# Optimization experiments

Hardware: AMD Instinct MI355X
Metric: run time of the kernel (lower is better)

The kernel has to match this reference:

```python
import jax, jax.numpy as jnp
import numpy as np

B, D, E, H = 2048, 1024, 32, 1024  # tokens, hidden, total experts (m*N), ffn_dim_small


def setup_inputs() -> dict:
    key = jax.random.key(0)
    ks = jax.random.split(key, 5)
    scale_in = 1.0 / np.sqrt(D)
    scale_h = 1.0 / np.sqrt(H)
    return {
        "x": jax.random.normal(ks[0], (B, D), dtype=jnp.float32),
        "Wg": jax.random.normal(ks[1], (D, E), dtype=jnp.float32) * scale_in,
        "W1": jax.random.normal(ks[2], (E, D, H), dtype=jnp.float32) * scale_in,
        "b1": jnp.zeros((E, H), dtype=jnp.float32),
        "W2": jax.random.normal(ks[3], (E, H, D), dtype=jnp.float32) * scale_h,
        "b2": jnp.zeros((E, D), dtype=jnp.float32),
        "topk": 8,  # m * K
    }


def reference(x, Wg, W1, b1, W2, b2, topk):
    # gating: softmax then keep only top-k probs (others zeroed), no renorm
    logits = x @ Wg                                   # [B, E]
    probs = jax.nn.softmax(logits, axis=-1)           # [B, E]
    _, idx = jax.lax.top_k(probs, topk)               # [B, topk]
    mask = jnp.zeros_like(probs).at[jnp.arange(x.shape[0])[:, None], idx].set(1.0)
    gate = probs * mask                               # [B, E]

    # dense all-expert FFN (faithful to original which runs every expert)
    h = jax.nn.relu(jnp.einsum('bd,edh->beh', x, W1) + b1)   # [B, E, H]
    y = jnp.einsum('beh,ehd->bed', h, W2) + b2               # [B, E, D]

    moe_out = jnp.einsum('be,bed->bd', gate, y)              # weighted sum over experts
    return x + moe_out
```

## Files before the change

### kernel.cpp

```cpp
#include <hip/hip_runtime.h>
#include <hip/hip_bf16.h>

#define B_TOK 2048
#define DDIM 1024
#define NEXP 32
#define HDIM 1024
#define TOPK 8
#define PITCH 1088

typedef __bf16 bf16_t;
typedef __bf16 bf16x8 __attribute__((ext_vector_type(8)));
typedef float f32x4 __attribute__((ext_vector_type(4)));

__global__ __launch_bounds__(256) void k_prep(const float* __restrict__ x,
                                              bf16_t* __restrict__ xb) {
  int i = (blockIdx.x * 256 + threadIdx.x) * 8;
  float4 v0 = *(const float4*)&x[i];
  float4 v1 = *(const float4*)&x[i + 4];
  bf16x8 v;
  v[0] = (bf16_t)v0.x; v[1] = (bf16_t)v0.y; v[2] = (bf16_t)v0.z; v[3] = (bf16_t)v0.w;
  v[4] = (bf16_t)v1.x; v[5] = (bf16_t)v1.y; v[6] = (bf16_t)v1.z; v[7] = (bf16_t)v1.w;
  int row = i >> 10, col = i & 1023;
  *(bf16x8*)&xb[(size_t)row * PITCH + col] = v;
}

__global__ __launch_bounds__(256) void k_gating(const float* __restrict__ x,
                                                const float* __restrict__ Wg,
                                                int* __restrict__ sel_e,
                                                float* __restrict__ sel_w) {
  int token = blockIdx.x * 4 + (threadIdx.x >> 6);
  int lane = threadIdx.x & 63;
  int e = lane & 31;
  int half = lane >> 5;
  const float* xr = x + (size_t)token * DDIM + half * (DDIM / 2);
  const float* wg = Wg + (size_t)half * (DDIM / 2) * NEXP + e;
  float acc = 0.f;
#pragma unroll 8
  for (int k = 0; k < DDIM / 2; ++k) acc = fmaf(xr[k], wg[k * NEXP], acc);
  acc += __shfl_xor(acc, 32);
  float m = acc;
  for (int off = 16; off; off >>= 1) m = fmaxf(m, __shfl_xor(m, off));
  float p = __expf(acc - m);
  float s = p;
  for (int off = 16; off; off >>= 1) s += __shfl_xor(s, off);
  p /= s;
  float pv = p;
  int my_se = 0;
  float my_sw = 0.f;
  for (int it = 0; it < TOPK; ++it) {
    float mx = pv;
    for (int off = 16; off; off >>= 1) mx = fmaxf(mx, __shfl_xor(mx, off));
    unsigned long long bal = __ballot(pv == mx);
    int sl = __ffsll(bal) - 1;
    int se = sl & 31;
    if (lane == it) { my_se = se; my_sw = mx; }
    if (e == se) pv = -1.f;
  }
  if (lane < TOPK) {
    sel_e[token * TOPK + lane] = my_se;
    sel_w[token * TOPK + lane] = my_sw;
  }
}

__global__ __launch_bounds__(256) void k_build_lists(const int* __restrict__ sel_e,
                                                     const float* __restrict__ sel_w,
                                                     int* __restrict__ list,
                                                     float* __restrict__ wlist,
                                                     int* __restrict__ count) {
  int e = blockIdx.x;
  int t = threadIdx.x;
  int lane = t & 63, wv = t >> 6;
  __shared__ int wsum[4];
  __shared__ int base;
  if (t == 0) base = 0;
  __syncthreads();
  for (int c = 0; c < B_TOK; c += 256) {
    int b = c + t;
    int flag = 0, slot = 0;
    float w = 0.f;
#pragma unroll
    for (int j = 0; j < TOPK; ++j) {
      if (sel_e[b * TOPK + j] == e) { flag = 1; slot = j; w = sel_w[b * TOPK + j]; }
    }
    unsigned long long bal = __ballot(flag);
    int pre = __popcll(bal & ((1ull << lane) - 1ull));
    int tot = __popcll(bal);
    if (lane == 0) wsum[wv] = tot;
    __syncthreads();
    int off = base;
    for (int i = 0; i < wv; ++i) off += wsum[i];
    if (flag) {
      int pos = off + pre;
      list[e * B_TOK + pos] = (b << 3) | slot;
      wlist[e * B_TOK + pos] = w;
    }
    __syncthreads();
    if (t == 0) base += wsum[0] + wsum[1] + wsum[2] + wsum[3];
    __syncthreads();
  }
  if (t == 0) count[e] = base;
}

__global__ __launch_bounds__(64) void k_build_queue(const int* __restrict__ count,
                                                    int* __restrict__ queue,
                                                    int* __restrict__ qn) {
  int e = threadIdx.x;
  int nmt = 0;
  if (e < NEXP) nmt = (count[e] + 127) >> 7;
  int pref = 0, tot = 0;
  for (int i = 0; i < NEXP; ++i) {
    int v = __shfl(nmt, i);
    if (i < e) pref += v;
    tot += v;
  }
  if (e < NEXP) {
    int base = pref * 8;
    for (int y = 0; y < 8; ++y)
      for (int mt = 0; mt < nmt; ++mt)
        queue[base + y * nmt + mt] = (e << 8) | (mt << 3) | y;
  }
  if (threadIdx.x == 0) qn[0] = tot * 8;
}

__global__ __launch_bounds__(256) void k_reduce(const float* __restrict__ x,
                                               const float* __restrict__ ybuf,
                                               float* __restrict__ out) {
  int i = (blockIdx.x * 256 + threadIdx.x) * 4;
  int tok = i >> 10;
  int d = i & 1023;
  float4 s = *(const float4*)&x[i];
  const float* yb = ybuf + (size_t)tok * 8 * 1024 + d;
#pragma unroll
  for (int sl = 0; sl < 8; ++sl) {
    float4 v = *(const float4*)&yb[sl * 1024];
    s.x += v.x; s.y += v.y; s.z += v.z; s.w += v.w;
  }
  *(float4*)&out[i] = s;
}

__device__ __forceinline__ void async_load16(const bf16_t* g, bf16_t* l) {
  __builtin_amdgcn_global_load_lds((const __attribute__((address_space(1))) void*)g,
                                   (__attribute__((address_space(3))) void*)l, 16, 0, 0);
}

#define LOADB(LO, HI, KT)                                                     \
  {                                                                           \
    const float* p_ = bcol + (size_t)((KT)*64 + aB * 8) * 1024;               \
    _Pragma("unroll") for (int kk = 0; kk < 8; ++kk) {                        \
      LO[kk] = *(const float2*)(p_ + (size_t)kk * 1024);                      \
      HI[kk] = *(const float2*)(p_ + (size_t)kk * 1024 + 64);                 \
    }                                                                         \
  }

#define CVTWRITE(LO, HI)                                                      \
  {                                                                           \
    _Pragma("unroll") for (int jn = 0; jn < 4; ++jn) {                        \
      const int n = (jn < 2) ? (2 * qB + jn) : (64 + 2 * qB + (jn - 2));      \
      bf16x8 pk;                                                              \
      _Pragma("unroll") for (int kk = 0; kk < 8; ++kk)                        \
          pk[kk] = (bf16_t)((jn == 0) ? LO[kk].x : (jn == 1) ? LO[kk].y       \
                            : (jn == 2) ? HI[kk].x : HI[kk].y);               \
      *(bf16x8*)&Bs[n][(aB ^ (n & 7)) << 3] = pk;                             \
    }                                                                         \
  }

#define ISSUE_A(KT)                                                           \
  {                                                                           \
    _Pragma("unroll") for (int i = 0; i < 4; ++i)                             \
        async_load16(aptr[i] + (KT)*64, &As[w * 32 + i * 8][0]);              \
  }

#define MFMA_PHASE()                                                          \
  {                                                                           \
    bf16x8 af[4][2], bfr[4][2];                                               \
    _Pragma("unroll") for (int ks = 0; ks < 2; ++ks) {                        \
      const int ca = (((ks << 2) | hi) ^ l7) << 3;                            \
      _Pragma("unroll") for (int m = 0; m < 4; ++m)                           \
          af[m][ks] = *(const bf16x8*)&As[wm + m * 16 + lr][ca];              \
      _Pragma("unroll") for (int n = 0; n < 4; ++n)                           \
          bfr[n][ks] = *(const bf16x8*)&Bs[wc + n * 16 + lr][ca];             \
    }                                                                         \
    _Pragma("unroll") for (int m = 0; m < 4; ++m)                             \
        _Pragma("unroll") for (int n = 0; n < 4; ++n)                         \
            _Pragma("unroll") for (int ks = 0; ks < 2; ++ks)                  \
                acc[m][n] = __builtin_amdgcn_mfma_f32_16x16x32_bf16(          \
                    af[m][ks], bfr[n][ks], acc[m][n], 0, 0, 0);               \
  }

template <int PHASE>
__global__ __launch_bounds__(256, 3) void k_gemm(const bf16_t* __restrict__ Abase,
                                                 const float* __restrict__ Wraw,
                                                 const int* __restrict__ list,
                                                 const float* __restrict__ wlist,
                                                 const int* __restrict__ count,
                                                 const int* __restrict__ queue,
                                                 const int* __restrict__ qn,
                                                 const float* __restrict__ bias,
                                                 bf16_t* __restrict__ hbuf,
                                                 float* __restrict__ ybuf) {
  __shared__ bf16_t As[128][64];
  __shared__ bf16_t Bs[128][64];

  const int phys = blockIdx.x;
  const int nwg = qn[0];
  if (phys >= nwg) return;
  const int q8 = nwg >> 3, r8 = nwg & 7;
  const int xcd = phys & 7, loc = phys >> 3;
  const int wk = (xcd < r8 ? xcd * (q8 + 1) : r8 * (q8 + 1) + (xcd - r8) * q8) + loc;

  const int ent = queue[wk];
  const int e = ent >> 8;
  const int mt = (ent >> 3) & 31;
  const int y = ent & 7;

  const int cnt = count[e];
  const int m0 = mt * 128;
  const int n0 = y * 128;

  const int t = threadIdx.x;
  const int lane = t & 63;
  const int w = t >> 6;
  const int wm = (w >> 1) << 6;
  const int wc = (w & 1) << 6;
  const int lr = lane & 15;
  const int hi = lane >> 4;
  const int l7 = lane & 7;
  const int srs = ((lane & 7) ^ (lane >> 3)) << 3;

  const int* lrow = list + e * B_TOK;

  const bf16_t* aptr[4];
#pragma unroll
  for (int i = 0; i < 4; ++i) {
    int mi = m0 + w * 32 + i * 8 + (lane >> 3);
    if (mi > cnt - 1) mi = cnt - 1;
    int li = lrow[mi];
    int tok = li >> 3, slot = li & 7;
    size_t arow = (PHASE == 1) ? (size_t)tok * PITCH : ((size_t)tok * 8 + slot) * PITCH;
    aptr[i] = Abase + arow + srs;
  }

  const int qB = t & 31;
  const int aB = t >> 5;
  const float* bcol = Wraw + (size_t)e * DDIM * HDIM + n0 + 2 * qB;

  f32x4 acc[4][4] = {};
  float2 valo[8], vahi[8], vblo[8], vbhi[8];

  LOADB(valo, vahi, 0)

#pragma unroll 1
  for (int kt2 = 0; kt2 < 8; ++kt2) {
    const int ktA = kt2 * 2;
    const int ktB = ktA + 1;
    ISSUE_A(ktA)
    CVTWRITE(valo, vahi)
    __syncthreads();
    LOADB(vblo, vbhi, ktB)
    MFMA_PHASE()
    __syncthreads();
    ISSUE_A(ktB)
    CVTWRITE(vblo, vbhi)
    __syncthreads();
    if (ktB < 15) LOADB(valo, vahi, ktB + 1)
    MFMA_PHASE()
    __syncthreads();
  }

  float biasv[4];
#pragma unroll
  for (int n = 0; n < 4; ++n) biasv[n] = bias[e * 1024 + n0 + wc + n * 16 + lr];

#pragma unroll
  for (int m = 0; m < 4; ++m) {
#pragma unroll
    for (int j = 0; j < 4; ++j) {
      int gm = m0 + wm + m * 16 + hi * 4 + j;
      if (gm < cnt) {
        int li2 = lrow[gm];
        int tok2 = li2 >> 3, slot2 = li2 & 7;
        if (PHASE == 1) {
          bf16_t* hr = hbuf + ((size_t)tok2 * 8 + slot2) * PITCH + n0 + wc + lr;
#pragma unroll
          for (int n = 0; n < 4; ++n) {
            float v = acc[m][n][j] + biasv[n];
            hr[n * 16] = (bf16_t)(v > 0.f ? v : 0.f);
          }
        } else {
          float gw = wlist[e * B_TOK + gm];
          float* yrow = ybuf + ((size_t)tok2 * 8 + slot2) * 1024 + n0 + wc + lr;
#pragma unroll
          for (int n = 0; n < 4; ++n) {
            yrow[n * 16] = (acc[m][n][j] + biasv[n]) * gw;
          }
        }
      }
    }
  }
}

extern "C" void kernel_launch(void* const* d_in, const int* in_sizes, int n_in,
                              void* d_out, int out_size, void* d_ws, size_t ws_size,
                              hipStream_t stream) {
  const float* x = (const float*)d_in[0];
  const float* Wg = (const float*)d_in[1];
  const float* W1 = (const float*)d_in[2];
  const float* b1 = (const float*)d_in[3];
  const float* W2 = (const float*)d_in[4];
  const float* b2 = (const float*)d_in[5];
  float* out = (float*)d_out;

  char* ws = (char*)d_ws;
  bf16_t* xb = (bf16_t*)ws;   ws += (size_t)B_TOK * PITCH * 2;
  bf16_t* hbuf = (bf16_t*)ws; ws += (size_t)B_TOK * TOPK * PITCH * 2;
  float* ybuf = (float*)ws;   ws += (size_t)B_TOK * TOPK * 1024 * 4;
  int* sel_e = (int*)ws;      ws += (size_t)B_TOK * TOPK * 4;
  float* sel_w = (float*)ws;  ws += (size_t)B_TOK * TOPK * 4;
  int* list = (int*)ws;       ws += (size_t)NEXP * B_TOK * 4;
  float* wlist = (float*)ws;  ws += (size_t)NEXP * B_TOK * 4;
  int* count = (int*)ws;      ws += 64 * 4;
  int* queue = (int*)ws;      ws += 2048 * 4;
  int* qn = (int*)ws;         ws += 64 * 4;

  k_prep<<<1024, 256, 0, stream>>>(x, xb);
  k_gating<<<512, 256, 0, stream>>>(x, Wg, sel_e, sel_w);
  k_build_lists<<<32, 256, 0, stream>>>(sel_e, sel_w, list, wlist, count);
  k_build_queue<<<1, 64, 0, stream>>>(count, queue, qn);
  k_gemm<1><<<1536, 256, 0, stream>>>(xb, W1, list, wlist, count, queue, qn, b1, hbuf, ybuf);
  k_gemm<2><<<1536, 256, 0, stream>>>(hbuf, W2, list, wlist, count, queue, qn, b2, hbuf, ybuf);
  k_reduce<<<2048, 256, 0, stream>>>(x, ybuf, out);
}
```

Measured before the change: 257.8 us.

## Double-buffer A tile in LDS and prefetch next A load during MFMA

Splits the A shared-memory tile into two buffers so the async global→LDS load of the next K-tile is issued before the current tile's MFMA phase rather than after it. The full __syncthreads barriers are replaced with an LDS-only waitcnt plus s_barrier, so outstanding global loads are not drained at every barrier. This aims to overlap A-operand memory latency with matrix math. It costs an extra 16KB of LDS per block. Correctness now depends on the in-order vector-memory wait that the compiler inserts for the B register loads also covering the earlier async A loads.

```diff
diff --git a/kernel.cpp b/kernel.cpp
--- a/kernel.cpp
+++ b/kernel.cpp
@@ -143,6 +143,9 @@
                                    (__attribute__((address_space(3))) void*)l, 16, 0, 0);
 }
 
+#define SYNCA asm volatile("s_waitcnt lgkmcnt(0)" ::: "memory"); __builtin_amdgcn_s_barrier();
+#define SYNCB asm volatile("s_waitcnt lgkmcnt(0)" ::: "memory"); __builtin_amdgcn_s_barrier();
+
 #define LOADB(LO, HI, KT)                                                     \
   {                                                                           \
     const float* p_ = bcol + (size_t)((KT)*64 + aB * 8) * 1024;               \
@@ -164,19 +167,19 @@
     }                                                                         \
   }
 
-#define ISSUE_A(KT)                                                           \
+#define ISSUE_A(KT, BUF)                                                      \
   {                                                                           \
     _Pragma("unroll") for (int i = 0; i < 4; ++i)                             \
-        async_load16(aptr[i] + (KT)*64, &As[w * 32 + i * 8][0]);              \
-  }
-
-#define MFMA_PHASE()                                                          \
+        async_load16(aptr[i] + (KT)*64, &As[BUF][w * 32 + i * 8][0]);         \
+  }
+
+#define MFMA_PHASE(BUF)                                                       \
   {                                                                           \
     bf16x8 af[4][2], bfr[4][2];                                               \
     _Pragma("unroll") for (int ks = 0; ks < 2; ++ks) {                        \
       const int ca = (((ks << 2) | hi) ^ l7) << 3;                            \
       _Pragma("unroll") for (int m = 0; m < 4; ++m)                           \
-          af[m][ks] = *(const bf16x8*)&As[wm + m * 16 + lr][ca];              \
+          af[m][ks] = *(const bf16x8*)&As[BUF][wm + m * 16 + lr][ca];         \
       _Pragma("unroll") for (int n = 0; n < 4; ++n)                           \
           bfr[n][ks] = *(const bf16x8*)&Bs[wc + n * 16 + lr][ca];             \
     }                                                                         \
@@ -198,7 +201,7 @@
                                                  const float* __restrict__ bias,
                                                  bf16_t* __restrict__ hbuf,
                                                  float* __restrict__ ybuf) {
-  __shared__ bf16_t As[128][64];
+  __shared__ bf16_t As[2][128][64];
   __shared__ bf16_t Bs[128][64];
 
   const int phys = blockIdx.x;
@@ -247,24 +250,27 @@
   f32x4 acc[4][4] = {};
   float2 valo[8], vahi[8], vblo[8], vbhi[8];
 
+  ISSUE_A(0, 0)
   LOADB(valo, vahi, 0)
 
 #pragma unroll 1
   for (int kt2 = 0; kt2 < 8; ++kt2) {
     const int ktA = kt2 * 2;
     const int ktB = ktA + 1;
-    ISSUE_A(ktA)
     CVTWRITE(valo, vahi)
-    __syncthreads();
+    SYNCA
+    ISSUE_A(ktB, 1)
     LOADB(vblo, vbhi, ktB)
-    MFMA_PHASE()
-    __syncthreads();
-    ISSUE_A(ktB)
+    MFMA_PHASE(0)
+    SYNCB
     CVTWRITE(vblo, vbhi)
-    __syncthreads();
-    if (ktB < 15) LOADB(valo, vahi, ktB + 1)
-    MFMA_PHASE()
-    __syncthreads();
+    SYNCA
+    if (ktB < 15) {
+      ISSUE_A(ktB + 1, 0)
+      LOADB(valo, vahi, ktB + 1)
+    }
+    MFMA_PHASE(1)
+    SYNCB
   }
 
   float biasv[4];
```

Measured after the change: 268.5 us. 1.04x slower.
